# Kernel tuning notes

Hardware: AMD Instinct MI355X
Metric: run time of the kernel (lower is better)

## Reference

```python
import jax, jax.numpy as jnp
import numpy as np

EMBED = 1024
HEADS = 16
HEAD_DIM = EMBED // HEADS


def setup_inputs() -> dict:
    key = jax.random.key(0)
    ks = jax.random.split(key, 12)
    B, S, D = 4, 2048, EMBED
    scale = 1.0 / np.sqrt(D)
    inp = {
        "query": jax.random.normal(ks[0], (B, S, D), dtype=jnp.float32),
        "key": jax.random.normal(ks[1], (B, S, D), dtype=jnp.float32),
        "value": jax.random.normal(ks[2], (B, S, D), dtype=jnp.float32),
        "Wq": jax.random.normal(ks[3], (D, D), dtype=jnp.float32) * scale,
        "bq": jnp.zeros((D,), dtype=jnp.float32),
        "Wk": jax.random.normal(ks[4], (D, D), dtype=jnp.float32) * scale,
        "bk": jnp.zeros((D,), dtype=jnp.float32),
        "Wv": jax.random.normal(ks[5], (D, D), dtype=jnp.float32) * scale,
        "bv": jnp.zeros((D,), dtype=jnp.float32),
        "Wo": jax.random.normal(ks[6], (D, D), dtype=jnp.float32) * scale,
        "bo": jnp.zeros((D,), dtype=jnp.float32),
    }
    return inp


def reference(query, key, value, Wq, bq, Wk, bk, Wv, bv, Wo, bo):
    B, S, D = query.shape
    H, Dh = HEADS, HEAD_DIM

    def proj(x, W, b):
        # nn.Linear: x @ W.T + b, then split heads -> [B, H, S, Dh]
        y = jnp.einsum('bsd,ed->bse', x, W) + b
        return y.reshape(B, -1, H, Dh).transpose(0, 2, 1, 3)

    q = proj(query, Wq, bq)
    k = proj(key, Wk, bk)
    v = proj(value, Wv, bv)

    attn = jnp.einsum('bhqd,bhkd->bhqk', q, k) / jnp.sqrt(jnp.float32(Dh))
    attn = jax.nn.softmax(attn, axis=-1)
    # dropout: eval mode -> identity
    out = jnp.einsum('bhqk,bhkd->bhqd', attn, v)
    out = out.transpose(0, 2, 1, 3).reshape(B, -1, D)
    out = jnp.einsum('bsd,ed->bse', out, Wo) + bo
    return out
```

## Files before the change

kernel.cpp:

```cpp
#include <hip/hip_runtime.h>
#include <hip/hip_bf16.h>

typedef unsigned short u16;
typedef unsigned int u32;
typedef float f32x4 __attribute__((ext_vector_type(4)));
typedef float f32x16 __attribute__((ext_vector_type(16)));
typedef __bf16 bf16x8 __attribute__((ext_vector_type(8)));
typedef u32 u32x2 __attribute__((ext_vector_type(2)));

#define DEV static __device__ __forceinline__

DEV u16 f2b(float f) { __bf16 h = (__bf16)f; u16 r; __builtin_memcpy(&r, &h, 2); return r; }
DEV u32 pk2(float a, float b) { return (u32)f2b(a) | ((u32)f2b(b) << 16); }
DEV bf16x8 as_bf(uint4 v) { bf16x8 r; __builtin_memcpy(&r, &v, 16); return r; }

#define GLDS(g, l) __builtin_amdgcn_global_load_lds( \
    (__attribute__((address_space(1))) void*)(g),     \
    (__attribute__((address_space(3))) void*)(l), 16, 0, 0)

__global__ __launch_bounds__(256) void conva_k(const float* __restrict__ src,
                                               u16* __restrict__ dst, int n8)
{
  int i = blockIdx.x * 256 + threadIdx.x;
  const int stride = gridDim.x * 256;
  for (; i < n8; i += stride) {
    const float4* p = (const float4*)(src + (size_t)i * 8);
    const float4 a = p[0], b = p[1];
    *(uint4*)(dst + (size_t)i * 8) =
        make_uint4(pk2(a.x, a.y), pk2(a.z, a.w), pk2(b.x, b.y), pk2(b.z, b.w));
  }
}

__global__ __launch_bounds__(256) void convw_k(const float* __restrict__ w0,
                                               const float* __restrict__ w1,
                                               const float* __restrict__ w2,
                                               const float* __restrict__ w3,
                                               u16* __restrict__ dst)
{
  const int seg = blockIdx.x >> 9, sb = blockIdx.x & 511;
  const float* s = seg == 0 ? w0 : seg == 1 ? w1 : seg == 2 ? w2 : w3;
  const int i = sb * 256 + threadIdx.x;
  const float4* p = (const float4*)(s + (size_t)i * 8);
  const float4 a = p[0], b = p[1];
  *(uint4*)(dst + (size_t)seg * 1048576 + (size_t)i * 8) =
      make_uint4(pk2(a.x, a.y), pk2(a.z, a.w), pk2(b.x, b.y), pk2(b.z, b.w));
}

template<int CMODE>
__global__ __launch_bounds__(512, 4) void gemm_b(const u16* __restrict__ A,
                                                 const u16* __restrict__ W,
                                                 const float* __restrict__ bias,
                                                 void* __restrict__ Cp, float scale)
{
  __shared__ u16 lds[2][8192];
  const int tid = threadIdx.x;
  const int lane = tid & 63, w = tid >> 6;
  const int m0 = blockIdx.x * 128, e0 = blockIdx.y * 128;
  const int wrb = (w >> 1) * 2, wcb = (w & 1) * 4;

  f32x4 acc[2][4];
#pragma unroll
  for (int i = 0; i < 2; i++)
#pragma unroll
    for (int j = 0; j < 4; j++)
#pragma unroll
      for (int r = 0; r < 4; r++) acc[i][j][r] = 0.f;

  const u16* gA = A + (size_t)(m0 + w * 16 + (lane & 15)) * 1024 + (lane >> 4) * 8;
  const u16* gB = W + (size_t)(e0 + w * 16 + (lane & 15)) * 1024 + (lane >> 4) * 8;

  GLDS(gA, &lds[0][w * 512]);
  GLDS(gB, &lds[0][4096 + w * 512]);
  __syncthreads();

  int buf = 0;
  const int fo = (lane >> 4) * 128 + (lane & 15) * 8;
  for (int kb = 0; kb < 32; ++kb) {
    const int nbuf = buf ^ 1;
    if (kb < 31) {
      const int k0 = (kb + 1) * 32;
      GLDS(gA + k0, &lds[nbuf][w * 512]);
      GLDS(gB + k0, &lds[nbuf][4096 + w * 512]);
    }
    const u16* la = &lds[buf][0];
    const u16* lb = &lds[buf][4096];
    bf16x8 af[2], bfr[4];
#pragma unroll
    for (int i = 0; i < 2; i++)
      af[i] = as_bf(*(const uint4*)(la + (wrb + i) * 512 + fo));
#pragma unroll
    for (int j = 0; j < 4; j++)
      bfr[j] = as_bf(*(const uint4*)(lb + (wcb + j) * 512 + fo));
#pragma unroll
    for (int i = 0; i < 2; i++)
#pragma unroll
      for (int j = 0; j < 4; j++)
        acc[i][j] = __builtin_amdgcn_mfma_f32_16x16x32_bf16(af[i], bfr[j], acc[i][j], 0, 0, 0);
    __syncthreads();
    buf = nbuf;
  }

  const int col = lane & 15, rb4 = (lane >> 4) * 4;
  const int wr = wrb * 16, wc = wcb * 16;
#pragma unroll
  for (int j = 0; j < 4; j++) {
    const int e = e0 + wc + j * 16 + col;
    const float bv = bias[e];
#pragma unroll
    for (int i = 0; i < 2; i++) {
#pragma unroll
      for (int r = 0; r < 4; r++) {
        const int m = m0 + wr + i * 16 + rb4 + r;
        const float v = (acc[i][j][r] + bv) * scale;
        if (CMODE == 0) {
          ((float*)Cp)[(size_t)m * 1024 + e] = v;
        } else {
          const int b = m >> 11, s = m & 2047, h = e >> 6, dh = e & 63;
          const size_t bh = (size_t)(b * 16 + h);
          if (CMODE == 2) {
            const size_t idx = (((bh * 64 + (s >> 5)) * 4 + (dh >> 4)) * 64
                                + ((dh >> 3) & 1) * 32 + (s & 31)) * 8 + (dh & 7);
            ((u16*)Cp)[idx] = f2b(v);
          } else {
            const size_t idx = ((bh * 64 + (s >> 5)) * 8 + ((s >> 4) & 1) * 4
                                + (dh >> 5) * 2 + ((s >> 3) & 1)) * 256
                               + (size_t)(dh & 31) * 8 + (s & 7);
            ((u16*)Cp)[idx] = f2b(v);
          }
        }
      }
    }
  }
}

__global__ __launch_bounds__(256, 4) void attn_k(const u16* __restrict__ Qb,
                                                 const u16* __restrict__ Kb,
                                                 const u16* __restrict__ Vb,
                                                 u16* __restrict__ O)
{
  __shared__ u16 kv[2][4096];
  __shared__ u16 ob[4][32][72];
  const int tid = threadIdx.x, wv = tid >> 6, lane = tid & 63;
  const int lo = lane & 31, hi = lane >> 5;
  const int bid = blockIdx.x;
  const int xcd = bid & 7, ix = bid >> 3;
  const int bh = xcd * 8 + (ix & 7);
  const int qb = (ix >> 3) * 4 + wv;
  const int b = bh >> 4, h = bh & 15, q0 = qb * 32;

  const u16* qp = Qb + ((size_t)(bh * 64 + qb) * 4) * 512 + (size_t)lane * 8;
  bf16x8 qf[4];
#pragma unroll
  for (int c = 0; c < 4; c++) qf[c] = as_bf(*(const uint4*)(qp + c * 512));

  const uint4 onesw = make_uint4(0x3F803F80u, 0x3F803F80u, 0x3F803F80u, 0x3F803F80u);
  const bf16x8 ones = as_bf(onesw);

  f32x16 a0, a1, a2, zv;
#pragma unroll
  for (int r = 0; r < 16; r++) { a0[r] = 0.f; a1[r] = 0.f; a2[r] = 0.f; zv[r] = 0.f; }

  const u16* sgK = Kb + (size_t)bh * 131072 + wv * 512 + (size_t)lane * 8;
  const u16* sgV = Vb + (size_t)bh * 131072 + wv * 512 + (size_t)lane * 8;

  GLDS(sgK, &kv[0][wv * 512]);
  GLDS(sgV, &kv[0][2048 + wv * 512]);
  __syncthreads();

#define ATTN_TILE(CUR, PT, DOPREF)                                            \
  {                                                                           \
    if (DOPREF) {                                                             \
      GLDS(sgK + (size_t)(PT) * 2048, &kv[(CUR) ^ 1][wv * 512]);              \
      GLDS(sgV + (size_t)(PT) * 2048, &kv[(CUR) ^ 1][2048 + wv * 512]);       \
    }                                                                         \
    const u16* kl = &kv[CUR][0];                                              \
    const u16* vl = &kv[CUR][2048];                                           \
    __builtin_amdgcn_s_setprio(1);                                            \
    f32x16 s = __builtin_amdgcn_mfma_f32_32x32x16_bf16(                       \
                 as_bf(*(const uint4*)(kl + lane * 8)), qf[0], zv, 0, 0, 0);  \
    _Pragma("unroll")                                                         \
    for (int c = 1; c < 4; c++)                                               \
      s = __builtin_amdgcn_mfma_f32_32x32x16_bf16(                            \
            as_bf(*(const uint4*)(kl + c * 512 + lane * 8)), qf[c], s, 0, 0, 0); \
    __builtin_amdgcn_s_setprio(0);                                            \
    _Pragma("unroll")                                                         \
    for (int r = 0; r < 16; r++) s[r] = __builtin_amdgcn_exp2f(s[r]);         \
    bf16x8 pf[2];                                                             \
    _Pragma("unroll")                                                         \
    for (int kc = 0; kc < 2; kc++) {                                          \
      const u32 A0 = pk2(s[8 * kc + 0], s[8 * kc + 1]);                       \
      const u32 A1 = pk2(s[8 * kc + 2], s[8 * kc + 3]);                       \
      const u32 B0 = pk2(s[8 * kc + 4], s[8 * kc + 5]);                       \
      const u32 B1 = pk2(s[8 * kc + 6], s[8 * kc + 7]);                       \
      u32x2 w02 = __builtin_amdgcn_permlane32_swap(A0, B0, false, false);     \
      u32x2 w13 = __builtin_amdgcn_permlane32_swap(A1, B1, false, false);     \
      pf[kc] = as_bf(make_uint4(w02[0], w13[0], w02[1], w13[1]));             \
    }                                                                         \
    __builtin_amdgcn_s_setprio(1);                                            \
    a0 = __builtin_amdgcn_mfma_f32_32x32x16_bf16(                             \
           as_bf(*(const uint4*)(vl + 0    + lane * 8)), pf[0], a0, 0, 0, 0); \
    a1 = __builtin_amdgcn_mfma_f32_32x32x16_bf16(                             \
           as_bf(*(const uint4*)(vl + 512  + lane * 8)), pf[0], a1, 0, 0, 0); \
    a2 = __builtin_amdgcn_mfma_f32_32x32x16_bf16(ones, pf[0], a2, 0, 0, 0);   \
    a0 = __builtin_amdgcn_mfma_f32_32x32x16_bf16(                             \
           as_bf(*(const uint4*)(vl + 1024 + lane * 8)), pf[1], a0, 0, 0, 0); \
    a1 = __builtin_amdgcn_mfma_f32_32x32x16_bf16(                             \
           as_bf(*(const uint4*)(vl + 1536 + lane * 8)), pf[1], a1, 0, 0, 0); \
    a2 = __builtin_amdgcn_mfma_f32_32x32x16_bf16(ones, pf[1], a2, 0, 0, 0);   \
    __builtin_amdgcn_s_setprio(0);                                            \
    __syncthreads();                                                          \
  }

  for (int t = 0; t < 64; t += 2) {
    ATTN_TILE(0, t + 1, 1)
    ATTN_TILE(1, t + 2, (t + 2 < 64))
  }
#undef ATTN_TILE

  const float inv = 1.f / a2[0];

#pragma unroll
  for (int r = 0; r < 16; r++) {
    const int dh = (r & 3) + 8 * (r >> 2) + 4 * hi;
    ob[wv][lo][dh]      = f2b(a0[r] * inv);
    ob[wv][lo][dh + 32] = f2b(a1[r] * inv);
  }
  const int qr = lane >> 1, hf = lane & 1;
  const u16* src = &ob[wv][qr][hf * 32];
  const uint4 r0 = *(const uint4*)(src + 0);
  const uint4 r1 = *(const uint4*)(src + 8);
  const uint4 r2 = *(const uint4*)(src + 16);
  const uint4 r3 = *(const uint4*)(src + 24);
  const size_t m = (size_t)b * 2048 + q0 + qr;
  uint4* dst = (uint4*)(O + m * 1024 + (size_t)h * 64 + hf * 32);
  dst[0] = r0; dst[1] = r1; dst[2] = r2; dst[3] = r3;
}

extern "C" void kernel_launch(void* const* d_in, const int* in_sizes, int n_in,
                              void* d_out, int out_size, void* d_ws, size_t ws_size,
                              hipStream_t stream)
{
  const float* query = (const float*)d_in[0];
  const float* key   = (const float*)d_in[1];
  const float* value = (const float*)d_in[2];
  const float* Wq = (const float*)d_in[3];
  const float* bq = (const float*)d_in[4];
  const float* Wk = (const float*)d_in[5];
  const float* bk = (const float*)d_in[6];
  const float* Wv = (const float*)d_in[7];
  const float* bv = (const float*)d_in[8];
  const float* Wo = (const float*)d_in[9];
  const float* bo = (const float*)d_in[10];

  const size_t MAT = (size_t)8192 * 1024;
  const size_t WMAT = (size_t)1024 * 1024;
  if (ws_size < (4 * MAT + 4 * WMAT) * sizeof(u16)) return;
  u16* Ac = (u16*)d_ws;
  u16* Wc = Ac + MAT;
  u16* Qw = Wc + 4 * WMAT;
  u16* Kw = Qw + MAT;
  u16* Vw = Kw + MAT;
  u16* Ow = Ac;

  const float qscale = 0.125f * 1.4426950408889634f;

  dim3 bl(256, 1, 1), bg(512, 1, 1), gg(64, 8);
  hipLaunchKernelGGL(convw_k, dim3(2048), bl, 0, stream, Wq, Wk, Wv, Wo, Wc);

  hipLaunchKernelGGL(conva_k, dim3(2048), bl, 0, stream, query, Ac, (int)(MAT / 8));
  hipLaunchKernelGGL((gemm_b<2>), gg, bg, 0, stream, Ac, Wc + 0 * WMAT, bq, (void*)Qw, qscale);

  hipLaunchKernelGGL(conva_k, dim3(2048), bl, 0, stream, key, Ac, (int)(MAT / 8));
  hipLaunchKernelGGL((gemm_b<2>), gg, bg, 0, stream, Ac, Wc + 1 * WMAT, bk, (void*)Kw, 1.0f);

  hipLaunchKernelGGL(conva_k, dim3(2048), bl, 0, stream, value, Ac, (int)(MAT / 8));
  hipLaunchKernelGGL((gemm_b<3>), gg, bg, 0, stream, Ac, Wc + 2 * WMAT, bv, (void*)Vw, 1.0f);

  hipLaunchKernelGGL(attn_k, dim3(1024), bl, 0, stream, Qw, Kw, Vw, Ow);

  hipLaunchKernelGGL((gemm_b<0>), gg, bg, 0, stream, Ow, Wc + 3 * WMAT, bo, d_out, 1.0f);
}
```

Baseline: 262.4 us.

## Triple-buffer LDS with partial vmcnt waits in GEMM and attention loops

```diff
diff --git a/kernel.cpp b/kernel.cpp
--- a/kernel.cpp
+++ b/kernel.cpp
@@ -17,6 +17,9 @@
 #define GLDS(g, l) __builtin_amdgcn_global_load_lds( \
     (__attribute__((address_space(1))) void*)(g),     \
     (__attribute__((address_space(3))) void*)(l), 16, 0, 0)
+
+DEV void wb2() { asm volatile("s_waitcnt vmcnt(2)\n\ts_barrier" ::: "memory"); }
+DEV void wb0() { asm volatile("s_waitcnt vmcnt(0)\n\ts_barrier" ::: "memory"); }
 
 __global__ __launch_bounds__(256) void conva_k(const float* __restrict__ src,
                                                u16* __restrict__ dst, int n8)
@@ -52,7 +55,7 @@
                                                  const float* __restrict__ bias,
                                                  void* __restrict__ Cp, float scale)
 {
-  __shared__ u16 lds[2][8192];
+  __shared__ u16 lds[3][8192];
   const int tid = threadIdx.x;
   const int lane = tid & 63, w = tid >> 6;
   const int m0 = blockIdx.x * 128, e0 = blockIdx.y * 128;
@@ -69,36 +72,45 @@
   const u16* gA = A + (size_t)(m0 + w * 16 + (lane & 15)) * 1024 + (lane >> 4) * 8;
   const u16* gB = W + (size_t)(e0 + w * 16 + (lane & 15)) * 1024 + (lane >> 4) * 8;
 
-  GLDS(gA, &lds[0][w * 512]);
-  GLDS(gB, &lds[0][4096 + w * 512]);
-  __syncthreads();
-
-  int buf = 0;
+  GLDS(gA,      &lds[0][w * 512]);
+  GLDS(gB,      &lds[0][4096 + w * 512]);
+  GLDS(gA + 32, &lds[1][w * 512]);
+  GLDS(gB + 32, &lds[1][4096 + w * 512]);
+
+  u16 *rc = &lds[0][0], *rn = &lds[1][0], *rf = &lds[2][0];
   const int fo = (lane >> 4) * 128 + (lane & 15) * 8;
-  for (int kb = 0; kb < 32; ++kb) {
-    const int nbuf = buf ^ 1;
-    if (kb < 31) {
-      const int k0 = (kb + 1) * 32;
-      GLDS(gA + k0, &lds[nbuf][w * 512]);
-      GLDS(gB + k0, &lds[nbuf][4096 + w * 512]);
+
+#define GEMM_STEP(KL)                                                          \
+  {                                                                            \
+    const u16* la = (KL);                                                      \
+    const u16* lb = (KL) + 4096;                                               \
+    bf16x8 af[2], bfr[4];                                                      \
+    _Pragma("unroll")                                                          \
+    for (int i = 0; i < 2; i++)                                                \
+      af[i] = as_bf(*(const uint4*)(la + (wrb + i) * 512 + fo));               \
+    _Pragma("unroll")                                                          \
+    for (int j = 0; j < 4; j++)                                                \
+      bfr[j] = as_bf(*(const uint4*)(lb + (wcb + j) * 512 + fo));              \
+    _Pragma("unroll")                                                          \
+    for (int i = 0; i < 2; i++)                                                \
+      _Pragma("unroll")                                                        \
+      for (int j = 0; j < 4; j++)                                              \
+        acc[i][j] = __builtin_amdgcn_mfma_f32_16x16x32_bf16(af[i], bfr[j],     \
+                                                            acc[i][j], 0, 0, 0); \
+  }
+
+  for (int kb = 0; kb < 31; ++kb) {
+    wb2();
+    if (kb < 30) {
+      GLDS(gA + (kb + 2) * 32, rf + w * 512);
+      GLDS(gB + (kb + 2) * 32, rf + 4096 + w * 512);
     }
-    const u16* la = &lds[buf][0];
-    const u16* lb = &lds[buf][4096];
-    bf16x8 af[2], bfr[4];
-#pragma unroll
-    for (int i = 0; i < 2; i++)
-      af[i] = as_bf(*(const uint4*)(la + (wrb + i) * 512 + fo));
-#pragma unroll
-    for (int j = 0; j < 4; j++)
-      bfr[j] = as_bf(*(const uint4*)(lb + (wcb + j) * 512 + fo));
-#pragma unroll
-    for (int i = 0; i < 2; i++)
-#pragma unroll
-      for (int j = 0; j < 4; j++)
-        acc[i][j] = __builtin_amdgcn_mfma_f32_16x16x32_bf16(af[i], bfr[j], acc[i][j], 0, 0, 0);
-    __syncthreads();
-    buf = nbuf;
-  }
+    GEMM_STEP(rc)
+    u16* tmp = rc; rc = rn; rn = rf; rf = tmp;
+  }
+  wb0();
+  GEMM_STEP(rc)
+#undef GEMM_STEP
 
   const int col = lane & 15, rb4 = (lane >> 4) * 4;
   const int wr = wrb * 16, wc = wcb * 16;
@@ -138,8 +150,7 @@
                                                  const u16* __restrict__ Vb,
                                                  u16* __restrict__ O)
 {
-  __shared__ u16 kv[2][4096];
-  __shared__ u16 ob[4][32][72];
+  __shared__ u16 pool[12288];
   const int tid = threadIdx.x, wv = tid >> 6, lane = tid & 63;
   const int lo = lane & 31, hi = lane >> 5;
   const int bid = blockIdx.x;
@@ -163,18 +174,17 @@
   const u16* sgK = Kb + (size_t)bh * 131072 + wv * 512 + (size_t)lane * 8;
   const u16* sgV = Vb + (size_t)bh * 131072 + wv * 512 + (size_t)lane * 8;
 
-  GLDS(sgK, &kv[0][wv * 512]);
-  GLDS(sgV, &kv[0][2048 + wv * 512]);
-  __syncthreads();
-
-#define ATTN_TILE(CUR, PT, DOPREF)                                            \
+  GLDS(sgK,        pool + wv * 512);
+  GLDS(sgV,        pool + 2048 + wv * 512);
+  GLDS(sgK + 2048, pool + 4096 + wv * 512);
+  GLDS(sgV + 2048, pool + 4096 + 2048 + wv * 512);
+
+  u16 *rc = pool, *rn = pool + 4096, *rf = pool + 8192;
+
+#define ATTN_STEP(KL)                                                         \
   {                                                                           \
-    if (DOPREF) {                                                             \
-      GLDS(sgK + (size_t)(PT) * 2048, &kv[(CUR) ^ 1][wv * 512]);              \
-      GLDS(sgV + (size_t)(PT) * 2048, &kv[(CUR) ^ 1][2048 + wv * 512]);       \
-    }                                                                         \
-    const u16* kl = &kv[CUR][0];                                              \
-    const u16* vl = &kv[CUR][2048];                                           \
+    const u16* kl = (KL);                                                     \
+    const u16* vl = (KL) + 2048;                                              \
     __builtin_amdgcn_s_setprio(1);                                            \
     f32x16 s = __builtin_amdgcn_mfma_f32_32x32x16_bf16(                       \
                  as_bf(*(const uint4*)(kl + lane * 8)), qf[0], zv, 0, 0, 0);  \
@@ -208,25 +218,35 @@
            as_bf(*(const uint4*)(vl + 1536 + lane * 8)), pf[1], a1, 0, 0, 0); \
     a2 = __builtin_amdgcn_mfma_f32_32x32x16_bf16(ones, pf[1], a2, 0, 0, 0);   \
     __builtin_amdgcn_s_setprio(0);                                            \
-    __syncthreads();                                                          \
-  }
-
-  for (int t = 0; t < 64; t += 2) {
-    ATTN_TILE(0, t + 1, 1)
-    ATTN_TILE(1, t + 2, (t + 2 < 64))
-  }
-#undef ATTN_TILE
+  }
+
+  for (int t = 0; t < 63; ++t) {
+    wb2();
+    if (t < 62) {
+      GLDS(sgK + (size_t)(t + 2) * 2048, rf + wv * 512);
+      GLDS(sgV + (size_t)(t + 2) * 2048, rf + 2048 + wv * 512);
+    }
+    ATTN_STEP(rc)
+    u16* tmp = rc; rc = rn; rn = rf; rf = tmp;
+  }
+  wb0();
+  ATTN_STEP(rc)
+#undef ATTN_STEP
+
+  __syncthreads();
 
   const float inv = 1.f / a2[0];
+  u16* ob = pool + (wv * 32) * 72;
 
 #pragma unroll
   for (int r = 0; r < 16; r++) {
     const int dh = (r & 3) + 8 * (r >> 2) + 4 * hi;
-    ob[wv][lo][dh]      = f2b(a0[r] * inv);
-    ob[wv][lo][dh + 32] = f2b(a1[r] * inv);
-  }
+    ob[lo * 72 + dh]      = f2b(a0[r] * inv);
+    ob[lo * 72 + dh + 32] = f2b(a1[r] * inv);
+  }
+  __builtin_amdgcn_s_barrier();
   const int qr = lane >> 1, hf = lane & 1;
-  const u16* src = &ob[wv][qr][hf * 32];
+  const u16* src = ob + qr * 72 + hf * 32;
   const uint4 r0 = *(const uint4*)(src + 0);
   const uint4 r1 = *(const uint4*)(src + 8);
   const uint4 r2 = *(const uint4*)(src + 16);
```

After: 262.8 us. No clear change (+0.1%).
